# Kernel tuning notes

Hardware: AMD Instinct MI355X
Metric: run time of the kernel (lower is better)

The kernel has to match this reference:

```python
import jax, jax.numpy as jnp
import numpy as np

B, S, D, H = 4, 2048, 1024, 16
DK = D // H


def setup_inputs() -> dict:
    key = jax.random.key(0)
    ks = jax.random.split(key, 11)
    s = 1.0 / np.sqrt(D)
    return {
        "Q": jax.random.normal(ks[0], (B, S, D), jnp.float32),
        "K": jax.random.normal(ks[1], (B, S, D), jnp.float32),
        "V": jax.random.normal(ks[2], (B, S, D), jnp.float32),
        "Wq": jax.random.normal(ks[3], (D, D), jnp.float32) * s,
        "bq": jnp.zeros((D,), jnp.float32),
        "Wk": jax.random.normal(ks[4], (D, D), jnp.float32) * s,
        "bk": jnp.zeros((D,), jnp.float32),
        "Wv": jax.random.normal(ks[5], (D, D), jnp.float32) * s,
        "bv": jnp.zeros((D,), jnp.float32),
        "Wo": jax.random.normal(ks[6], (D, D), jnp.float32) * s,
        "bo": jnp.zeros((D,), jnp.float32),
    }


def reference(Q, K, V, Wq, bq, Wk, bk, Wv, bv, Wo, bo):
    # projections: [B,S,D] -> [B,H,S,DK]
    def split_heads(x):
        return x.reshape(B, -1, H, DK).transpose(0, 2, 1, 3)

    q = split_heads(Q @ Wq.T + bq)
    k = split_heads(K @ Wk.T + bk)
    v = split_heads(V @ Wv.T + bv)
    scale = 1.0 / jnp.sqrt(jnp.float32(DK))
    scores = jnp.einsum("bhqd,bhkd->bhqk", q, k) * scale
    attn = jax.nn.softmax(scores, axis=-1)  # dropout = identity (eval)
    out = jnp.einsum("bhqk,bhkd->bhqd", attn, v)
    out = out.transpose(0, 2, 1, 3).reshape(B, -1, D)
    return out @ Wo.T + bo
```

## Files before the change

kernel.cpp:

```cpp
#include <hip/hip_runtime.h>

#define SEQ    2048
#define DMODEL 1024
#define NH     16
#define DKH    64
#define MROWS  8192

typedef unsigned short u16;
typedef __bf16    bf16x8 __attribute__((ext_vector_type(8)));
typedef _Float16  f16x4  __attribute__((ext_vector_type(4)));
typedef _Float16  f16x8  __attribute__((ext_vector_type(8)));
typedef __fp16    hf16x2 __attribute__((ext_vector_type(2)));
typedef float     f32x4  __attribute__((ext_vector_type(4)));
typedef u16       u16x4  __attribute__((ext_vector_type(4)));
typedef u16       u16x8  __attribute__((ext_vector_type(8)));

__device__ __forceinline__ u16 f2b(float f) {
  union { float f; unsigned u; } v; v.f = f;
  unsigned r = v.u + 0x7fffu + ((v.u >> 16) & 1u);
  return (u16)(r >> 16);
}
__device__ __forceinline__ unsigned pk_f16(float a, float b) {
  union { hf16x2 h; unsigned u; } v;
  v.h = __builtin_amdgcn_cvt_pkrtz(a, b);
  return v.u;
}

__global__ __launch_bounds__(256) void cvt3_kernel(
    const float* __restrict__ a0, const float* __restrict__ a1, const float* __restrict__ a2,
    u16* o0, u16* o1, u16* o2, int n4) {
  int i = blockIdx.x * 256 + threadIdx.x;
  if (i >= n4) return;
  const float* in; u16* out;
  switch (blockIdx.y) {
    case 0: in = a0; out = o0; break;
    case 1: in = a1; out = o1; break;
    default: in = a2; out = o2; break;
  }
  f32x4 v = ((const f32x4*)in)[i];
  u16x4 o;
  o.x = f2b(v.x); o.y = f2b(v.y); o.z = f2b(v.z); o.w = f2b(v.w);
  ((u16x4*)out)[i] = o;
}
__global__ __launch_bounds__(256) void cvt4_kernel(
    const float* __restrict__ a0, const float* __restrict__ a1,
    const float* __restrict__ a2, const float* __restrict__ a3,
    u16* o0, u16* o1, u16* o2, u16* o3, int n4) {
  int i = blockIdx.x * 256 + threadIdx.x;
  if (i >= n4) return;
  const float* in; u16* out;
  switch (blockIdx.y) {
    case 0: in = a0; out = o0; break;
    case 1: in = a1; out = o1; break;
    case 2: in = a2; out = o2; break;
    default: in = a3; out = o3; break;
  }
  f32x4 v = ((const f32x4*)in)[i];
  u16x4 o;
  o.x = f2b(v.x); o.y = f2b(v.y); o.z = f2b(v.z); o.w = f2b(v.w);
  ((u16x4*)out)[i] = o;
}

__device__ __forceinline__ void gemm_body(
    const u16* __restrict__ A, const u16* __restrict__ W,
    const float* __restrict__ bias, void* __restrict__ outp, int mode, float oscale,
    int bx, int by, u16* smem) {
  const int tid  = threadIdx.x;
  const int w    = tid >> 6;
  const int lane = tid & 63;
  const int l15  = lane & 15;
  const int quad = lane >> 4;
  const int x7   = l15 & 7;
  const int n0 = bx * 128;
  const int m0 = by * 128;
  const int wm = (w >> 1) * 64;
  const int wn = (w & 1) * 64;

  f32x4 acc[4][4];
#pragma unroll
  for (int mt = 0; mt < 4; ++mt)
#pragma unroll
    for (int nt = 0; nt < 4; ++nt)
      acc[mt][nt] = (f32x4){0.f, 0.f, 0.f, 0.f};

  const int srow = w * 32 + (lane >> 3);
  const int scol = (((lane & 7) ^ (lane >> 3)) * 8);
  const size_t arow = (size_t)(m0 + srow) * DMODEL;
  const size_t brow = (size_t)(n0 + srow) * DMODEL;

  auto stage = [&](int buf, int ks) {
    u16* Asb = smem + buf * 16384;
    u16* Bsb = Asb + 8192;
    const int k0 = ks * 64;
#pragma unroll
    for (int i = 0; i < 4; ++i) {
      __builtin_amdgcn_global_load_lds(
          (const __attribute__((address_space(1))) void*)(A + arow + (size_t)i * 8 * DMODEL + k0 + scol),
          (__attribute__((address_space(3))) void*)(&Asb[(w * 4 + i) * 512]),
          16, 0, 0);
      __builtin_amdgcn_global_load_lds(
          (const __attribute__((address_space(1))) void*)(W + brow + (size_t)i * 8 * DMODEL + k0 + scol),
          (__attribute__((address_space(3))) void*)(&Bsb[(w * 4 + i) * 512]),
          16, 0, 0);
    }
  };

  stage(0, 0);
  int cur = 0;

  for (int ks = 0; ks < DMODEL / 64; ++ks) {
    if (ks + 1 < DMODEL / 64) {
      stage(cur ^ 1, ks + 1);
      asm volatile("s_waitcnt vmcnt(8)" ::: "memory");
    } else {
      asm volatile("s_waitcnt vmcnt(0)" ::: "memory");
    }
    __builtin_amdgcn_s_barrier();

    const u16* As = smem + cur * 16384;
    const u16* Bs = As + 8192;
#pragma unroll
    for (int kk = 0; kk < 64; kk += 32) {
      const int kc = kk >> 3;
      bf16x8 af[4], bfr[4];
#pragma unroll
      for (int mt = 0; mt < 4; ++mt) {
        const int row = wm + mt * 16 + l15;
        af[mt] = *(const bf16x8*)&As[row * 64 + (((kc + quad) ^ (row & 7)) * 8)];
      }
#pragma unroll
      for (int nt = 0; nt < 4; ++nt) {
        const int row = wn + nt * 16 + l15;
        bfr[nt] = *(const bf16x8*)&Bs[row * 64 + (((kc + quad) ^ (row & 7)) * 8)];
      }
#pragma unroll
      for (int mt = 0; mt < 4; ++mt)
#pragma unroll
        for (int nt = 0; nt < 4; ++nt)
          acc[mt][nt] = __builtin_amdgcn_mfma_f32_16x16x32_bf16(af[mt], bfr[nt], acc[mt][nt], 0, 0, 0);
    }

    asm volatile("" ::: "memory");
    __builtin_amdgcn_s_barrier();
    cur ^= 1;
  }

  if (mode == 3) {
    float* o = (float*)outp;
#pragma unroll
    for (int nt = 0; nt < 4; ++nt) {
      const int col = n0 + wn + nt * 16 + l15;
      const float bv = bias[col];
#pragma unroll
      for (int mt = 0; mt < 4; ++mt) {
        const int mbase = m0 + wm + mt * 16 + quad * 4;
        f32x4 c = acc[mt][nt];
#pragma unroll
        for (int r = 0; r < 4; ++r)
          o[(size_t)(mbase + r) * DMODEL + col] = (c[r] + bv) * oscale;
      }
    }
    return;
  }

  u16* Cs = smem;
  if (mode == 0) {
#pragma unroll
    for (int nt = 0; nt < 4; ++nt) {
      const int col = n0 + wn + nt * 16 + l15;
      const float bv = bias[col];
      const int nl = wn + nt * 16 + l15;
      const int n8 = nl >> 3;
#pragma unroll
      for (int mt = 0; mt < 4; ++mt) {
        const int mb = wm + mt * 16 + quad * 4;
        f32x4 c = acc[mt][nt];
#pragma unroll
        for (int r = 0; r < 4; ++r) {
          const int m = mb + r;
          Cs[m * 128 + ((n8 ^ (m & 7)) * 8) + x7] = f2b((c[r] + bv) * oscale);
        }
      }
    }
  } else {
#pragma unroll
    for (int nt = 0; nt < 4; ++nt) {
      const int col = n0 + wn + nt * 16 + l15;
      const float bv = bias[col];
      const int nl = wn + nt * 16 + l15;
#pragma unroll
      for (int mt = 0; mt < 4; ++mt) {
        const int mb = wm + mt * 16 + quad * 4;
        f32x4 c = acc[mt][nt];
        union { u16x4 u4; unsigned u2[2]; } pk;
        pk.u2[0] = pk_f16((c[0] + bv) * oscale, (c[1] + bv) * oscale);
        pk.u2[1] = pk_f16((c[2] + bv) * oscale, (c[3] + bv) * oscale);
        *(u16x4*)&Cs[nl * 128 + (((mb >> 3) ^ (nl & 7)) * 8) + (mb & 7)] = pk.u4;
      }
    }
  }
  __syncthreads();

  const int rl   = tid >> 1;
  const int half = tid & 1;
  const int b    = m0 >> 11;
  if (mode == 0) {
    u16* o = (u16*)outp;
    const int s = (m0 + rl) & 2047;
    const int h = (n0 >> 6) + half;
    u16* orow = o + (((size_t)(b * NH + h) * SEQ + s)) * DKH;
#pragma unroll
    for (int j = 0; j < 8; ++j) {
      u16x8 v = *(const u16x8*)&Cs[rl * 128 + (((half * 8 + j) ^ (rl & 7)) * 8)];
      *(u16x8*)&orow[j * 8] = v;
    }
  } else {
    u16* o = (u16*)outp;
    const int plane = b * 1024 + n0 + rl;
    const int scol2 = (m0 & 2047) + half * 64;
    u16* orow = o + (size_t)plane * SEQ + scol2;
#pragma unroll
    for (int j = 0; j < 8; ++j) {
      u16x8 v = *(const u16x8*)&Cs[rl * 128 + (((half * 8 + j) ^ (rl & 7)) * 8)];
      *(u16x8*)&orow[j * 8] = v;
    }
  }
}

__device__ __forceinline__ void xcd_remap(int& bx, int& by) {
  const int lin = (int)blockIdx.x + (int)blockIdx.y * 8;
  const int xcd = lin & 7;
  const int idx = lin >> 3;
  by = xcd * 8 + (idx >> 3);
  bx = idx & 7;
}

__global__ __launch_bounds__(256) void gemm_kernel(
    const u16* __restrict__ A, const u16* __restrict__ W,
    const float* __restrict__ bias, void* __restrict__ outp, int mode, float oscale) {
  __shared__ __align__(16) u16 smem[32768];
  int bx, by; xcd_remap(bx, by);
  gemm_body(A, W, bias, outp, mode, oscale, bx, by, smem);
}

__global__ __launch_bounds__(256) void qkv_gemm_kernel(
    const u16* Aq, const u16* Ak, const u16* Av,
    const u16* Wq, const u16* Wk, const u16* Wv,
    const float* bq, const float* bk, const float* bv,
    u16* oq, u16* ok, u16* ov, float qscale) {
  __shared__ __align__(16) u16 smem[32768];
  const u16* A; const u16* W; const float* bias; u16* o; int mode; float sc;
  switch (blockIdx.z) {
    case 0:  A = Aq; W = Wq; bias = bq; o = oq; mode = 0; sc = qscale; break;
    case 1:  A = Ak; W = Wk; bias = bk; o = ok; mode = 0; sc = 1.f;    break;
    default: A = Av; W = Wv; bias = bv; o = ov; mode = 2; sc = 1.f;    break;
  }
  int bx, by; xcd_remap(bx, by);
  gemm_body(A, W, bias, o, mode, sc, bx, by, smem);
}

__global__ __launch_bounds__(128, 2) void attn_kernel(
    const u16* __restrict__ qh, const u16* __restrict__ kh,
    const u16* __restrict__ vt, u16* __restrict__ ao) {
  __shared__ __align__(16) u16 smem[16384];

  const int tid  = threadIdx.x;
  const int w    = tid >> 6;
  const int lane = tid & 63;
  const int l15  = lane & 15;
  const int quad = lane >> 4;
  const int x7   = l15 & 7;

  const int lin = (int)blockIdx.x + ((int)blockIdx.y << 4);
  const int bh  = (lin & 7) * 8 + ((lin >> 3) >> 4);
  const int q0  = ((lin >> 3) & 15) * 128;

  const u16* kbase = kh + (size_t)bh * SEQ * DKH;
  const u16* vbase = vt + (size_t)bh * DKH * SEQ;

  const int lr  = lane >> 3;
  const int lc8 = ((lane & 7) ^ lr) * 8;

  const int rbase = l15 * 64;
  const int c0 = (quad ^ x7) * 8;
  const int c1 = c0 ^ 32;

  bf16x8 qf[4][2];
#pragma unroll
  for (int g = 0; g < 4; ++g) {
    const u16* qrow = qh + ((size_t)bh * SEQ + q0 + w * 64 + g * 16 + l15) * DKH;
    qf[g][0] = *(const bf16x8*)(qrow + quad * 8);
    qf[g][1] = *(const bf16x8*)(qrow + 32 + quad * 8);
  }
#pragma unroll
  for (int g = 0; g < 4; ++g) {
    asm volatile("" : "+v"(qf[g][0]));
    asm volatile("" : "+v"(qf[g][1]));
  }
  asm volatile("s_waitcnt vmcnt(0)" ::: "memory");

  auto stage = [&](int buf, int k0) {
    u16* Ksb = smem + buf * 8192;
    u16* Vsb = Ksb + 4096;
#pragma unroll
    for (int i = 0; i < 4; ++i) {
      const int rowb = i * 16 + w * 8;
      const int krow = rowb + lr;
      const int kkey = ((krow >> 4) & 1) * 32 + ((krow >> 2) & 3) * 8 +
                       (krow >> 5) * 4 + (krow & 3);
      __builtin_amdgcn_global_load_lds(
          (const __attribute__((address_space(1))) void*)(kbase + (size_t)(k0 + kkey) * DKH + lc8),
          (__attribute__((address_space(3))) void*)(&Ksb[rowb * 64]), 16, 0, 0);
      __builtin_amdgcn_global_load_lds(
          (const __attribute__((address_space(1))) void*)(vbase + (size_t)(rowb + lr) * SEQ + k0 + lc8),
          (__attribute__((address_space(3))) void*)(&Vsb[rowb * 64]), 16, 0, 0);
    }
  };

  f32x4 o[4][4];
#pragma unroll
  for (int g = 0; g < 4; ++g)
#pragma unroll
    for (int dt = 0; dt < 4; ++dt) o[g][dt] = (f32x4){0.f, 0.f, 0.f, 0.f};
  float lsum[4] = {0.f, 0.f, 0.f, 0.f};

  stage(0, 0);
  int cur = 0;

  for (int kt = 0; kt < SEQ / 64; ++kt) {
    if (kt + 1 < SEQ / 64) {
      stage(cur ^ 1, (kt + 1) * 64);
      asm volatile("s_waitcnt vmcnt(8)" ::: "memory");
    } else {
      asm volatile("s_waitcnt vmcnt(0)" ::: "memory");
    }
    __builtin_amdgcn_s_barrier();

    const u16* Ks = smem + cur * 8192;
    const u16* Vs = Ks + 4096;

    bf16x8 kf[4][2];
#pragma unroll
    for (int nt = 0; nt < 4; ++nt) {
      kf[nt][0] = *(const bf16x8*)&Ks[nt * 1024 + rbase + c0];
      kf[nt][1] = *(const bf16x8*)&Ks[nt * 1024 + rbase + c1];
    }

    f16x8 pb[4][2];
#pragma unroll
    for (int g = 0; g < 4; ++g) {
      f32x4 sf[4];
      __builtin_amdgcn_s_setprio(1);
#pragma unroll
      for (int nt = 0; nt < 4; ++nt) {
        f32x4 a = (f32x4){-8.f, -8.f, -8.f, -8.f};
        a = __builtin_amdgcn_mfma_f32_16x16x32_bf16(kf[nt][0], qf[g][0], a, 0, 0, 0);
        a = __builtin_amdgcn_mfma_f32_16x16x32_bf16(kf[nt][1], qf[g][1], a, 0, 0, 0);
        sf[nt] = a;
      }
      __builtin_amdgcn_s_setprio(0);
      unsigned d0[4], d1[4];
#pragma unroll
      for (int nt = 0; nt < 4; ++nt) {
        float p0 = __builtin_amdgcn_exp2f(sf[nt][0]);
        float p1 = __builtin_amdgcn_exp2f(sf[nt][1]);
        float p2 = __builtin_amdgcn_exp2f(sf[nt][2]);
        float p3 = __builtin_amdgcn_exp2f(sf[nt][3]);
        lsum[g] += (p0 + p1) + (p2 + p3);
        d0[nt] = pk_f16(p0, p1);
        d1[nt] = pk_f16(p2, p3);
      }
#pragma unroll
      for (int b2 = 0; b2 < 2; ++b2) {
        union { f16x8 h; unsigned u[4]; } u;
        u.u[0] = d0[b2]; u.u[1] = d1[b2]; u.u[2] = d0[b2 + 2]; u.u[3] = d1[b2 + 2];
        pb[g][b2] = u.h;
      }
    }

    __builtin_amdgcn_s_setprio(1);
#pragma unroll
    for (int dt = 0; dt < 4; ++dt) {
#pragma unroll
      for (int b2 = 0; b2 < 2; ++b2) {
        const int vaddr = (dt * 16 + l15) * 64 + (((b2 * 4 + quad) ^ x7) * 8);
        f16x8 vf = *(const f16x8*)&Vs[vaddr];
#pragma unroll
        for (int g = 0; g < 4; ++g)
          o[g][dt] = __builtin_amdgcn_mfma_f32_16x16x32_f16(vf, pb[g][b2], o[g][dt], 0, 0, 0);
      }
    }
    __builtin_amdgcn_s_setprio(0);

    asm volatile("" ::: "memory");
    __builtin_amdgcn_s_barrier();
    cur ^= 1;
  }

  float inv[4];
#pragma unroll
  for (int g = 0; g < 4; ++g) {
    float l = lsum[g];
    l += __shfl_xor(l, 16);
    l += __shfl_xor(l, 32);
    inv[g] = 1.0f / l;
  }

  __syncthreads();
#pragma unroll
  for (int g = 0; g < 4; ++g) {
    const int q = w * 64 + g * 16 + l15;
#pragma unroll
    for (int dt = 0; dt < 4; ++dt) {
      const int dk = dt * 16 + quad * 4;
      u16x4 pk;
      pk.x = f2b(o[g][dt][0] * inv[g]);
      pk.y = f2b(o[g][dt][1] * inv[g]);
      pk.z = f2b(o[g][dt][2] * inv[g]);
      pk.w = f2b(o[g][dt][3] * inv[g]);
      *(u16x4*)&smem[q * 64 + (((dk >> 3) ^ (q & 7)) * 8) + (dk & 7)] = pk;
    }
  }
  __syncthreads();

  const int b = bh >> 4;
  const int h = bh & 15;
  const int rr = tid >> 3;
  const int cc = tid & 7;
#pragma unroll
  for (int j = 0; j < 8; ++j) {
    const int row = j * 16 + rr;
    u16x8 v = *(const u16x8*)&smem[row * 64 + ((cc ^ (row & 7)) * 8)];
    u16* orow = ao + ((size_t)(b * SEQ + q0 + row)) * DMODEL + h * DKH + cc * 8;
    *(u16x8*)orow = v;
  }
}

extern "C" void kernel_launch(void* const* d_in, const int* in_sizes, int n_in,
                              void* d_out, int out_size, void* d_ws, size_t ws_size,
                              hipStream_t stream) {
  const float* Q  = (const float*)d_in[0];
  const float* K  = (const float*)d_in[1];
  const float* V  = (const float*)d_in[2];
  const float* Wq = (const float*)d_in[3];
  const float* bq = (const float*)d_in[4];
  const float* Wk = (const float*)d_in[5];
  const float* bk = (const float*)d_in[6];
  const float* Wv = (const float*)d_in[7];
  const float* bv = (const float*)d_in[8];
  const float* Wo = (const float*)d_in[9];
  const float* bo = (const float*)d_in[10];

  const float QSCALE = 0.18033688011112042f;
  char* ws = (char*)d_ws;
  const size_t MB = 1ull << 20;
  const int nA4 = (MROWS * DMODEL) / 4;
  const int nW4 = (DMODEL * DMODEL) / 4;
  dim3 gg(DMODEL / 128, MROWS / 128);
  dim3 ag(SEQ / 128, 4 * NH);

  if (ws_size >= 104 * MB) {
    u16* Xq  = (u16*)(ws);
    u16* Xk  = (u16*)(ws + 16 * MB);
    u16* Xv  = (u16*)(ws + 32 * MB);
    u16* Wqb = (u16*)(ws + 48 * MB);
    u16* Wkb = (u16*)(ws + 50 * MB);
    u16* Wvb = (u16*)(ws + 52 * MB);
    u16* Wob = (u16*)(ws + 54 * MB);
    u16* qh  = (u16*)(ws + 56 * MB);
    u16* kh  = (u16*)(ws + 72 * MB);
    u16* vth = (u16*)(ws + 88 * MB);
    u16* AO  = Xq;

    cvt4_kernel<<<dim3(nW4 / 256, 4), 256, 0, stream>>>(Wq, Wk, Wv, Wo, Wqb, Wkb, Wvb, Wob, nW4);
    cvt3_kernel<<<dim3(nA4 / 256, 3), 256, 0, stream>>>(Q, K, V, Xq, Xk, Xv, nA4);
    qkv_gemm_kernel<<<dim3(8, 64, 3), 256, 0, stream>>>(
        Xq, Xk, Xv, Wqb, Wkb, Wvb, bq, bk, bv, qh, kh, vth, QSCALE);
    attn_kernel<<<ag, 128, 0, stream>>>(qh, kh, vth, AO);
    gemm_kernel<<<gg, 256, 0, stream>>>(AO, Wob, bo, d_out, 3, 1.0f);
  } else {
    u16* X   = (u16*)(ws);
    u16* Wqb = (u16*)(ws + 16 * MB);
    u16* Wkb = (u16*)(ws + 18 * MB);
    u16* Wvb = (u16*)(ws + 20 * MB);
    u16* Wob = (u16*)(ws + 22 * MB);
    u16* qh  = (u16*)(ws + 24 * MB);
    u16* kh  = (u16*)(ws + 40 * MB);
    u16* vth = (u16*)(ws + 56 * MB);

    cvt4_kernel<<<dim3(nW4 / 256, 4), 256, 0, stream>>>(Wq, Wk, Wv, Wo, Wqb, Wkb, Wvb, Wob, nW4);
    cvt3_kernel<<<dim3(nA4 / 256, 1), 256, 0, stream>>>(Q, Q, Q, X, X, X, nA4);
    gemm_kernel<<<gg, 256, 0, stream>>>(X, Wqb, bq, qh, 0, QSCALE);
    cvt3_kernel<<<dim3(nA4 / 256, 1), 256, 0, stream>>>(K, K, K, X, X, X, nA4);
    gemm_kernel<<<gg, 256, 0, stream>>>(X, Wkb, bk, kh, 0, 1.0f);
    cvt3_kernel<<<dim3(nA4 / 256, 1), 256, 0, stream>>>(V, V, V, X, X, X, nA4);
    gemm_kernel<<<gg, 256, 0, stream>>>(X, Wvb, bv, vth, 2, 1.0f);
    attn_kernel<<<ag, 128, 0, stream>>>(qh, kh, vth, X);
    gemm_kernel<<<gg, 256, 0, stream>>>(X, Wob, bo, d_out, 3, 1.0f);
  }
}
```

Measured before the change: 333.9 us.

## Fuse fp32-to-bf16 activation conversion into QKV projection GEMM loads

Removes the separate cvt3 pass over Q, K and V. The QKV GEMM now reads fp32 activations directly into registers, converts them to bf16, and writes them to shared memory, with the next tile's loads software-pipelined. This avoids writing and then re-reading 48MB of bf16 intermediates. In exchange, the A tile is read as fp32 and reloaded by each of the 8 N-column blocks, so those re-reads move twice the bytes. The register-staged A path also adds VGPR pressure and conversion ALU work inside the main loop.

Result: slower. 370.4 us (+10.9%).

```diff
diff --git a/kernel.cpp b/kernel.cpp
--- a/kernel.cpp
+++ b/kernel.cpp
@@ -5,6 +5,7 @@
 #define NH     16
 #define DKH    64
 #define MROWS  8192
+
 
 typedef unsigned short u16;
 typedef __bf16    bf16x8 __attribute__((ext_vector_type(8)));
@@ -227,6 +228,167 @@
   }
 }
 
+__device__ __forceinline__ void gemm_body_f32a(
+    const float* __restrict__ A, const u16* __restrict__ W,
+    const float* __restrict__ bias, u16* __restrict__ outp, int mode, float oscale,
+    int bx, int by, u16* smem) {
+  const int tid  = threadIdx.x;
+  const int w    = tid >> 6;
+  const int lane = tid & 63;
+  const int l15  = lane & 15;
+  const int quad = lane >> 4;
+  const int x7   = l15 & 7;
+  const int n0 = bx * 128;
+  const int m0 = by * 128;
+  const int wm = (w >> 1) * 64;
+  const int wn = (w & 1) * 64;
+
+  f32x4 acc[4][4];
+#pragma unroll
+  for (int mt = 0; mt < 4; ++mt)
+#pragma unroll
+    for (int nt = 0; nt < 4; ++nt)
+      acc[mt][nt] = (f32x4){0.f, 0.f, 0.f, 0.f};
+
+  const int srow = w * 32 + (lane >> 3);
+  const int scol = (((lane & 7) ^ (lane >> 3)) * 8);
+  const size_t arow = (size_t)(m0 + srow) * DMODEL;
+  const size_t brow = (size_t)(n0 + srow) * DMODEL;
+
+  f32x4 alo[4], ahi[4];
+  auto loadA = [&](int ks) {
+    const int k0 = ks * 64;
+#pragma unroll
+    for (int i = 0; i < 4; ++i) {
+      const float* p = A + arow + (size_t)i * 8 * DMODEL + k0 + scol;
+      alo[i] = *(const f32x4*)p;
+      ahi[i] = *(const f32x4*)(p + 4);
+    }
+  };
+  auto stageB = [&](int buf, int ks) {
+    u16* Bsb = smem + buf * 16384 + 8192;
+    const int k0 = ks * 64;
+#pragma unroll
+    for (int i = 0; i < 4; ++i) {
+      __builtin_amdgcn_global_load_lds(
+          (const __attribute__((address_space(1))) void*)(W + brow + (size_t)i * 8 * DMODEL + k0 + scol),
+          (__attribute__((address_space(3))) void*)(&Bsb[(w * 4 + i) * 512]),
+          16, 0, 0);
+    }
+  };
+  auto writeA = [&](int buf) {
+    u16* Asb = smem + buf * 16384;
+#pragma unroll
+    for (int i = 0; i < 4; ++i) {
+      u16x8 v;
+      v[0] = f2b(alo[i][0]); v[1] = f2b(alo[i][1]);
+      v[2] = f2b(alo[i][2]); v[3] = f2b(alo[i][3]);
+      v[4] = f2b(ahi[i][0]); v[5] = f2b(ahi[i][1]);
+      v[6] = f2b(ahi[i][2]); v[7] = f2b(ahi[i][3]);
+      *(u16x8*)&Asb[(w * 4 + i) * 512 + lane * 8] = v;
+    }
+  };
+
+  loadA(0);
+  stageB(0, 0);
+  writeA(0);
+  __syncthreads();
+  int cur = 0;
+
+  for (int ks = 0; ks < DMODEL / 64; ++ks) {
+    if (ks + 1 < DMODEL / 64) {
+      loadA(ks + 1);
+      stageB(cur ^ 1, ks + 1);
+    }
+    const u16* As = smem + cur * 16384;
+    const u16* Bs = As + 8192;
+#pragma unroll
+    for (int kk = 0; kk < 64; kk += 32) {
+      const int kc = kk >> 3;
+      bf16x8 af[4], bfr[4];
+#pragma unroll
+      for (int mt = 0; mt < 4; ++mt) {
+        const int row = wm + mt * 16 + l15;
+        af[mt] = *(const bf16x8*)&As[row * 64 + (((kc + quad) ^ (row & 7)) * 8)];
+      }
+#pragma unroll
+      for (int nt = 0; nt < 4; ++nt) {
+        const int row = wn + nt * 16 + l15;
+        bfr[nt] = *(const bf16x8*)&Bs[row * 64 + (((kc + quad) ^ (row & 7)) * 8)];
+      }
+#pragma unroll
+      for (int mt = 0; mt < 4; ++mt)
+#pragma unroll
+        for (int nt = 0; nt < 4; ++nt)
+          acc[mt][nt] = __builtin_amdgcn_mfma_f32_16x16x32_bf16(af[mt], bfr[nt], acc[mt][nt], 0, 0, 0);
+    }
+    if (ks + 1 < DMODEL / 64) writeA(cur ^ 1);
+    __syncthreads();
+    cur ^= 1;
+  }
+
+  u16* Cs = smem;
+  if (mode == 0) {
+#pragma unroll
+    for (int nt = 0; nt < 4; ++nt) {
+      const int col = n0 + wn + nt * 16 + l15;
+      const float bv = bias[col];
+      const int nl = wn + nt * 16 + l15;
+      const int n8 = nl >> 3;
+#pragma unroll
+      for (int mt = 0; mt < 4; ++mt) {
+        const int mb = wm + mt * 16 + quad * 4;
+        f32x4 c = acc[mt][nt];
+#pragma unroll
+        for (int r = 0; r < 4; ++r) {
+          const int m = mb + r;
+          Cs[m * 128 + ((n8 ^ (m & 7)) * 8) + x7] = f2b((c[r] + bv) * oscale);
+        }
+      }
+    }
+  } else {
+#pragma unroll
+    for (int nt = 0; nt < 4; ++nt) {
+      const int col = n0 + wn + nt * 16 + l15;
+      const float bv = bias[col];
+      const int nl = wn + nt * 16 + l15;
+#pragma unroll
+      for (int mt = 0; mt < 4; ++mt) {
+        const int mb = wm + mt * 16 + quad * 4;
+        f32x4 c = acc[mt][nt];
+        union { u16x4 u4; unsigned u2[2]; } pk;
+        pk.u2[0] = pk_f16((c[0] + bv) * oscale, (c[1] + bv) * oscale);
+        pk.u2[1] = pk_f16((c[2] + bv) * oscale, (c[3] + bv) * oscale);
+        *(u16x4*)&Cs[nl * 128 + (((mb >> 3) ^ (nl & 7)) * 8) + (mb & 7)] = pk.u4;
+      }
+    }
+  }
+  __syncthreads();
+
+  const int rl   = tid >> 1;
+  const int half = tid & 1;
+  const int b    = m0 >> 11;
+  if (mode == 0) {
+    const int s = (m0 + rl) & 2047;
+    const int h = (n0 >> 6) + half;
+    u16* orow = outp + (((size_t)(b * NH + h) * SEQ + s)) * DKH;
+#pragma unroll
+    for (int j = 0; j < 8; ++j) {
+      u16x8 v = *(const u16x8*)&Cs[rl * 128 + (((half * 8 + j) ^ (rl & 7)) * 8)];
+      *(u16x8*)&orow[j * 8] = v;
+    }
+  } else {
+    const int plane = b * 1024 + n0 + rl;
+    const int scol2 = (m0 & 2047) + half * 64;
+    u16* orow = outp + (size_t)plane * SEQ + scol2;
+#pragma unroll
+    for (int j = 0; j < 8; ++j) {
+      u16x8 v = *(const u16x8*)&Cs[rl * 128 + (((half * 8 + j) ^ (rl & 7)) * 8)];
+      *(u16x8*)&orow[j * 8] = v;
+    }
+  }
+}
+
 __device__ __forceinline__ void xcd_remap(int& bx, int& by) {
   const int lin = (int)blockIdx.x + (int)blockIdx.y * 8;
   const int xcd = lin & 7;
@@ -241,6 +403,22 @@
   __shared__ __align__(16) u16 smem[32768];
   int bx, by; xcd_remap(bx, by);
   gemm_body(A, W, bias, outp, mode, oscale, bx, by, smem);
+}
+
+__global__ __launch_bounds__(256) void qkv_gemm_f32a_kernel(
+    const float* Aq, const float* Ak, const float* Av,
+    const u16* Wq, const u16* Wk, const u16* Wv,
+    const float* bq, const float* bk, const float* bv,
+    u16* oq, u16* ok, u16* ov, float qscale) {
+  __shared__ __align__(16) u16 smem[32768];
+  const float* A; const u16* W; const float* bias; u16* o; int mode; float sc;
+  switch (blockIdx.z) {
+    case 0:  A = Aq; W = Wq; bias = bq; o = oq; mode = 0; sc = qscale; break;
+    case 1:  A = Ak; W = Wk; bias = bk; o = ok; mode = 0; sc = 1.f;    break;
+    default: A = Av; W = Wv; bias = bv; o = ov; mode = 2; sc = 1.f;    break;
+  }
+  int bx, by; xcd_remap(bx, by);
+  gemm_body_f32a(A, W, bias, o, mode, sc, bx, by, smem);
 }
 
 __global__ __launch_bounds__(256) void qkv_gemm_kernel(
@@ -460,22 +638,18 @@
   dim3 ag(SEQ / 128, 4 * NH);
 
   if (ws_size >= 104 * MB) {
-    u16* Xq  = (u16*)(ws);
-    u16* Xk  = (u16*)(ws + 16 * MB);
-    u16* Xv  = (u16*)(ws + 32 * MB);
-    u16* Wqb = (u16*)(ws + 48 * MB);
-    u16* Wkb = (u16*)(ws + 50 * MB);
-    u16* Wvb = (u16*)(ws + 52 * MB);
-    u16* Wob = (u16*)(ws + 54 * MB);
-    u16* qh  = (u16*)(ws + 56 * MB);
-    u16* kh  = (u16*)(ws + 72 * MB);
-    u16* vth = (u16*)(ws + 88 * MB);
-    u16* AO  = Xq;
+    u16* Wqb = (u16*)(ws);
+    u16* Wkb = (u16*)(ws + 2 * MB);
+    u16* Wvb = (u16*)(ws + 4 * MB);
+    u16* Wob = (u16*)(ws + 6 * MB);
+    u16* qh  = (u16*)(ws + 8 * MB);
+    u16* kh  = (u16*)(ws + 24 * MB);
+    u16* vth = (u16*)(ws + 40 * MB);
+    u16* AO  = (u16*)(ws + 56 * MB);
 
     cvt4_kernel<<<dim3(nW4 / 256, 4), 256, 0, stream>>>(Wq, Wk, Wv, Wo, Wqb, Wkb, Wvb, Wob, nW4);
-    cvt3_kernel<<<dim3(nA4 / 256, 3), 256, 0, stream>>>(Q, K, V, Xq, Xk, Xv, nA4);
-    qkv_gemm_kernel<<<dim3(8, 64, 3), 256, 0, stream>>>(
-        Xq, Xk, Xv, Wqb, Wkb, Wvb, bq, bk, bv, qh, kh, vth, QSCALE);
+    qkv_gemm_f32a_kernel<<<dim3(8, 64, 3), 256, 0, stream>>>(
+        Q, K, V, Wqb, Wkb, Wvb, bq, bk, bv, qh, kh, vth, QSCALE);
     attn_kernel<<<ag, 128, 0, stream>>>(qh, kh, vth, AO);
     gemm_kernel<<<gg, 256, 0, stream>>>(AO, Wob, bo, d_out, 3, 1.0f);
   } else {
```
